# Optimization experiments

Hardware: AMD Instinct MI355X
Metric: run time of the kernel (lower is better)

The kernel has to match this reference:

```python
import jax, jax.numpy as jnp
import numpy as np

B, C3, H3, W3 = 8, 512, 24, 24
C5, H5, W5 = 256, 96, 96
GRIDS = (6, 3, 2, 1)
GROUPS = 2


def conv2d(x, w):
    # stride-1 'same' conv (matches torch autopad k//2 for odd k), NCHW/OIHW
    return jax.lax.conv_general_dilated(x, w, (1, 1), 'SAME',
                                        dimension_numbers=('NCHW', 'OIHW', 'NCHW'))


def conv_bn_silu(x, w):
    # ultralytics-style Conv = Conv2d(bias=False) + BatchNorm2d + SiLU.
    # BN in eval with default running stats (mean=0, var=1, gamma=1, beta=0) is identity.
    return jax.nn.silu(conv2d(x, w))


def psp(x):
    # adaptive_avg_pool2d to (g, g) for each grid; H,W divisible by all grids -> equal bins
    b, c, h, w = x.shape
    outs = []
    for g in GRIDS:
        outs.append(x.reshape(b, c, g, h // g, g, w // g).mean(axis=(3, 5)).reshape(b, c, g * g))
    return jnp.concatenate(outs, axis=2)  # [b, c, 36+9+4+1=50]


def resize_bilinear_ac(x, oh, ow):
    # F.interpolate(mode='bilinear', align_corners=True)
    n, c, h, w = x.shape
    ys = jnp.linspace(0.0, h - 1.0, oh)
    xs = jnp.linspace(0.0, w - 1.0, ow)
    y0 = jnp.clip(jnp.floor(ys).astype(jnp.int32), 0, h - 2)
    x0 = jnp.clip(jnp.floor(xs).astype(jnp.int32), 0, w - 2)
    wy = (ys - y0)[None, None, :, None]
    wx = (xs - x0)[None, None, None, :]
    xr = jnp.take(x, y0, axis=2) * (1 - wy) + jnp.take(x, y0 + 1, axis=2) * wy
    return jnp.take(xr, x0, axis=3) * (1 - wx) + jnp.take(xr, x0 + 1, axis=3) * wx


def grid_sample(img, grid):
    # F.grid_sample bilinear, align_corners=True, padding_mode='zeros'
    # img [N,C,H,W], grid [N,Ho,Wo,2] with (x,y) normalized coords
    n, c, h, w = img.shape
    gx = (grid[..., 0] + 1.0) * 0.5 * (w - 1)
    gy = (grid[..., 1] + 1.0) * 0.5 * (h - 1)
    x0 = jnp.floor(gx)
    y0 = jnp.floor(gy)
    wx1 = gx - x0
    wy1 = gy - y0
    flat = img.reshape(n, c, h * w)

    def gather(xi, yi, wgt):
        valid = (xi >= 0) & (xi <= w - 1) & (yi >= 0) & (yi <= h - 1)
        xc = jnp.clip(xi, 0, w - 1).astype(jnp.int32)
        yc = jnp.clip(yi, 0, h - 1).astype(jnp.int32)
        idx = (yc * w + xc).reshape(n, 1, -1)
        v = jnp.take_along_axis(flat, idx, axis=2).reshape(n, c, grid.shape[1], grid.shape[2])
        return v * (wgt * valid)[:, None]

    return (gather(x0, y0, (1 - wx1) * (1 - wy1)) + gather(x0 + 1, y0, wx1 * (1 - wy1))
            + gather(x0, y0 + 1, (1 - wx1) * wy1) + gather(x0 + 1, y0 + 1, wx1 * wy1))


def _w(key, shape):
    fan_in = int(np.prod(shape[1:]))
    return (jax.random.normal(key, shape, jnp.float32) / np.sqrt(fan_in)).astype(jnp.float32)


def setup_inputs() -> dict:
    key = jax.random.key(0)
    ks = jax.random.split(key, 17)
    return {
        'p3': jax.random.normal(ks[0], (B, C3, H3, W3), jnp.float32),
        'p5': jax.random.normal(ks[1], (B, C5, H5, W5), jnp.float32),
        # CFC_CRB
        'w_red': _w(ks[2], (C3, C3, 3, 3)),
        'wq': _w(ks[3], (32, C3, 1, 1)), 'bq': jnp.zeros((32,), jnp.float32),
        'wk': _w(ks[4], (32, C3)), 'bk': jnp.zeros((32,), jnp.float32),
        'wv': _w(ks[5], (C3, C3)), 'bv': jnp.zeros((C3,), jnp.float32),
        'la_w1': _w(ks[6], (C3 // 8, C3, 1, 1)),
        'la_w2': _w(ks[7], (C3, C3 // 8, 3, 3)),
        # SFC_G2
        'w32': _w(ks[8], (C5, C3, 3, 3)),
        'w8': _w(ks[9], (C5, C5, 3, 3)),
        'woff1': _w(ks[10], (64, 2 * C5, 1, 1)),
        'woff2': _w(ks[11], (GROUPS * 4 + 2, 64, 3, 3)),
    }


def reference(p3, p5, w_red, wq, bq, wk, bk, wv, bv, la_w1, la_w2, w32, w8, woff1, woff2):
    # ---------------- CFC_CRB ----------------
    x = conv_bn_silu(p3, w_red)                      # [b,512,h,w]
    b, c, h, w = x.shape
    q = conv2d(x, wq) + bq[None, :, None, None]       # [b,32,h,w]
    q = q.reshape(b, 32, h * w).transpose(0, 2, 1)    # [b,N,32]
    kfeat = psp(x)                                    # [b,512,50]
    k = jnp.einsum('oc,bcm->bom', wk, kfeat) + bk[None, :, None]   # [b,32,50]
    sim = jax.nn.softmax(jnp.einsum('bnc,bcm->bnm', q, k), axis=-1)  # [b,N,50]
    v = jnp.einsum('oc,bcm->bom', wv, kfeat) + bv[None, :, None]   # [b,512,50]
    context = jnp.einsum('bcm,bnm->bcn', v, sim).reshape(b, c, h, w)
    # LocalAttenModule: res1 * tanh(conv(context)) + res2
    mask = jnp.tanh(conv2d(conv_bn_silu(context, la_w1), la_w2))
    context = context * mask + context
    p3o = x + context                                 # [b,512,24,24]

    # ---------------- SFC_G2 ----------------
    sp = conv_bn_silu(p3o, w32)                       # [b,256,24,24]
    sp = resize_bilinear_ac(sp, H5, W5)               # [b,256,96,96]
    cp = conv_bn_silu(p5, w8)                         # [b,256,96,96]
    cr = conv2d(conv_bn_silu(jnp.concatenate([cp, sp], axis=1), woff1), woff2)  # [b,10,96,96]

    n = b
    spg = sp.reshape(n * GROUPS, -1, H5, W5)
    cpg = cp.reshape(n * GROUPS, -1, H5, W5)
    off_l = cr[:, 0:GROUPS * 2].reshape(n * GROUPS, 2, H5, W5)
    off_h = cr[:, GROUPS * 2:GROUPS * 4].reshape(n * GROUPS, 2, H5, W5)

    gx = jnp.linspace(-1.0, 1.0, W5)
    gy = jnp.linspace(-1.0, 1.0, H5)
    X, Y = jnp.meshgrid(gx, gy)                       # [H5,W5] each
    base = jnp.stack([X, Y], axis=-1)[None]           # [1,H5,W5,2] (x,y)
    norm = jnp.array([W5, H5], dtype=sp.dtype)
    grid_l = base + off_l.transpose(0, 2, 3, 1) / norm
    grid_h = base + off_h.transpose(0, 2, 3, 1) / norm

    cps = grid_sample(cpg, grid_l).reshape(n, -1, H5, W5)
    sps = grid_sample(spg, grid_h).reshape(n, -1, H5, W5)
    att = 1.0 + jnp.tanh(cr[:, GROUPS * 4:])          # [b,2,H,W]
    p5o = sps * att[:, 0:1] + cps * att[:, 1:2]
    return (p3o, p5o)
```

## Files before the change

kernel.cpp:

```cpp
#include <hip/hip_runtime.h>
#include <math.h>

#define DI __device__ __forceinline__

typedef __attribute__((ext_vector_type(8))) short bf16x8;
typedef __attribute__((ext_vector_type(4))) float f32x4;

DI float silu_f(float v) { return v / (1.f + __expf(-v)); }
DI float4 ld4(const float* p) { return *reinterpret_cast<const float4*>(p); }
DI void st4(float* p, const float4& v) { *reinterpret_cast<float4*>(p) = v; }
DI unsigned short f2bf(float f) {
    unsigned u = __float_as_uint(f);
    unsigned r = (u + 0x7FFFu + ((u >> 16) & 1u)) >> 16;
    return (unsigned short)r;
}
DI float bf2f(unsigned short u) { return __uint_as_float(((unsigned)u) << 16); }

DI void gload_lds16(const unsigned short* g, unsigned short* l) {
    __builtin_amdgcn_global_load_lds(
        (const __attribute__((address_space(1))) void*)g,
        (__attribute__((address_space(3))) void*)l, 16, 0, 0);
}

__global__ void pack_w2_kernel(const float* __restrict__ w, unsigned short* __restrict__ pk,
                               int Ci, int Co, int COG) {
    int idx = blockIdx.x * 256 + threadIdx.x;
    int total = Ci * Co * 9;
    if (idx >= total) return;
    int cc = idx & 31;
    int t = idx >> 5;
    int col = t % COG; t /= COG;
    int dydx = t % 9;  t /= 9;
    int nCoG = Co / COG;
    int cog = t % nCoG;
    int ch = t / nCoG;
    int co = cog * COG + col;
    pk[idx] = f2bf(w[((size_t)co * Ci + (ch << 5) + cc) * 9 + dydx]);
}

__global__ void pack_w1_kernel(const float* __restrict__ w, unsigned short* __restrict__ pk) {
    int idx = blockIdx.x * 256 + threadIdx.x;
    if (idx >= 32768) return;
    int cc = idx & 31;
    int col = (idx >> 5) & 63;
    int ch = idx >> 11;
    pk[idx] = f2bf(w[(size_t)col * 512 + (ch << 5) + cc]);
}

__global__ void pack_in_pad_kernel(const float* __restrict__ in, unsigned short* __restrict__ pk,
                                   int Ci, int H, int W, int total) {
    int idx = blockIdx.x * 256 + threadIdx.x;
    if (idx >= total) return;
    const int nCh = Ci >> 5;
    const int HW = H * W;
    int cg = idx & 3;
    int t = idx >> 2;
    int pix = t % HW; t /= HW;
    int ch = t % nCh;
    int b = t / nCh;
    int y = pix / W, x = pix % W;
    const float* src = in + ((size_t)b * Ci + (ch << 5) + (cg << 3)) * HW + pix;
    unsigned p[4];
#pragma unroll
    for (int j = 0; j < 4; ++j) {
        float v0 = src[(size_t)(2 * j) * HW];
        float v1 = src[(size_t)(2 * j + 1) * HW];
        p[j] = (unsigned)f2bf(v0) | ((unsigned)f2bf(v1) << 16);
    }
    size_t dst = (((size_t)b * nCh + ch) * (H + 2) + (y + 1)) * (W + 2) + (x + 1);
    *(uint4*)&pk[dst * 32 + (cg << 3)] = make_uint4(p[0], p[1], p[2], p[3]);
}

template <int TH, int TW, int BF, int WCO, int FUSE, int OUTPK, int OUTPAD>
__global__ void __launch_bounds__(256)
conv3x3_mfma3(const unsigned short* __restrict__ pin, const unsigned short* __restrict__ wpk,
              float* __restrict__ out, unsigned short* __restrict__ outpk,
              int B, int Ci, int Co, int H, int W,
              const float* __restrict__ ctx, const float* __restrict__ xres) {
    static_assert(TH * TW == 4 * BF * 16, "tile px = 4 waves * BF frags * 16");
    constexpr int COG = WCO * 16;
    constexpr int TWH = TW + 2;
    constexpr int HP = (TH + 2) * TWH;
    constexpr int NG = HP * 4;
    constexpr int NIT = (NG + 255) / 256;
    static_assert(NG % 8 == 0, "granules divisible by 8");
    __shared__ __align__(16) unsigned short linA[NG * 8];

    const int nTx = W / TW, nTy = H / TH, nCoG = Co / COG;
    const int Wp = W + 2, Hp = H + 2;
    const int nwg = gridDim.x;
    int wg = (blockIdx.x & 7) * (nwg >> 3) + (blockIdx.x >> 3);
    const int cog = wg % nCoG; wg /= nCoG;
    const int tx = wg % nTx;   wg /= nTx;
    const int ty = wg % nTy;
    const int b = wg / nTy;
    const int ox = tx * TW, oy = ty * TH, co0 = cog * COG;

    const int tid = threadIdx.x;
    const int lane = tid & 63;
    const int l15 = lane & 15, g = lane >> 4;
    const int wpx = (tid >> 6) * (BF * 16);

    int rr[BF], cc_[BF];
#pragma unroll
    for (int bf = 0; bf < BF; ++bf) {
        int px = wpx + bf * 16 + l15;
        rr[bf] = px / TW;
        cc_[bf] = px % TW;
    }

    f32x4 acc[WCO][BF];
#pragma unroll
    for (int af = 0; af < WCO; ++af)
#pragma unroll
        for (int bf = 0; bf < BF; ++bf) acc[af][bf] = {};

    const int nCh = Ci >> 5;
    const size_t HWs = (size_t)H * W;

    for (int ch = 0; ch < nCh; ++ch) {
        {
            const unsigned short* srcb =
                pin + ((size_t)b * nCh + ch) * (size_t)Hp * Wp * 32;
#pragma unroll
            for (int it = 0; it < NIT; ++it) {
                int s = it * 256 + tid;
                if (s < NG) {
                    int e = s ^ ((s >> 3) & 7);
                    int hp = e >> 2, cgp = e & 3;
                    int hy = hp / TWH, hx = hp - hy * TWH;
                    gload_lds16(srcb + ((size_t)(oy + hy) * Wp + (ox + hx)) * 32
                                     + (cgp << 3),
                                &linA[(s & ~63) << 3]);
                }
            }
        }
        __syncthreads();

        {
            const unsigned short* wbase =
                wpk + ((((size_t)ch * nCoG + cog) * 9) * COG + l15) * 32 + (g << 3);
#pragma unroll
            for (int dy = 0; dy < 3; ++dy) {
#pragma unroll
                for (int dx = 0; dx < 3; ++dx) {
                    const int dydx = dy * 3 + dx;
                    bf16x8 a[WCO];
#pragma unroll
                    for (int af = 0; af < WCO; ++af)
                        a[af] = *(const bf16x8*)(wbase + ((size_t)dydx * COG + af * 16) * 32);
                    bf16x8 bb[BF];
#pragma unroll
                    for (int bf = 0; bf < BF; ++bf) {
                        int pxh = (rr[bf] + dy) * TWH + cc_[bf] + dx;
                        int eg = (pxh << 2) | g;
                        int slot = eg ^ ((eg >> 3) & 7);
                        bb[bf] = *(const bf16x8*)&linA[slot << 3];
                    }
#pragma unroll
                    for (int af = 0; af < WCO; ++af)
#pragma unroll
                        for (int bf = 0; bf < BF; ++bf)
                            acc[af][bf] = __builtin_amdgcn_mfma_f32_16x16x32_bf16(
                                a[af], bb[bf], acc[af][bf], 0, 0, 0);
                }
            }
        }
        __syncthreads();
    }

    const int nChO = Co >> 5;
    const size_t opitch = OUTPAD ? (size_t)(H + 2) * (W + 2) : HWs;
#pragma unroll
    for (int af = 0; af < WCO; ++af) {
#pragma unroll
        for (int bf = 0; bf < BF; ++bf) {
            int px = wpx + bf * 16 + l15;
            int y = oy + px / TW, x = ox + px % TW;
            size_t pixg = (size_t)y * W + x;
            int coB = co0 + af * 16 + (g << 2);
            float vv[4];
#pragma unroll
            for (int r4 = 0; r4 < 4; ++r4) {
                float v = acc[af][bf][r4];
                if (FUSE == 1) v = silu_f(v);
                else if (FUSE == 2) {
                    size_t base = ((size_t)b * Co + coB + r4) * HWs + pixg;
                    v = xres[base] + ctx[base] * (1.f + tanhf(v));
                }
                vv[r4] = v;
            }
            if (OUTPK != 1) {
#pragma unroll
                for (int r4 = 0; r4 < 4; ++r4)
                    out[((size_t)b * Co + coB + r4) * HWs + pixg] = vv[r4];
            }
            if (OUTPK >= 1) {
                ushort4 s;
                s.x = f2bf(vv[0]); s.y = f2bf(vv[1]); s.z = f2bf(vv[2]); s.w = f2bf(vv[3]);
                size_t opix = OUTPAD ? ((size_t)(y + 1) * (W + 2) + (x + 1)) : pixg;
                *(ushort4*)&outpk[(((size_t)b * nChO + (coB >> 5)) * opitch + opix) * 32
                                  + (coB & 31)] = s;
            }
        }
    }
}

__global__ void __launch_bounds__(256)
cat_mfma(const unsigned short* __restrict__ cp_pk, const unsigned short* __restrict__ sp_pk,
         const unsigned short* __restrict__ wpk, float* __restrict__ out) {
    __shared__ __align__(16) unsigned short lin1[128 * 36];
    const int nwg = gridDim.x;
    int wg = (blockIdx.x & 7) * (nwg >> 3) + (blockIdx.x >> 3);
    int mt = wg % 72;
    int b = wg / 72;
    int m0 = mt * 128;
    const int tid = threadIdx.x;
    const int wave = tid >> 6, lane = tid & 63;
    const int l15 = lane & 15, g = lane >> 4;
    const int wpx = wave * 32;

    f32x4 acc[4][2];
#pragma unroll
    for (int af = 0; af < 4; ++af)
#pragma unroll
        for (int bf = 0; bf < 2; ++bf) acc[af][bf] = {};

    for (int ch = 0; ch < 16; ++ch) {
        const unsigned short* src = (ch < 8)
            ? cp_pk + (((size_t)b * 8 + ch) * 9216 + m0) * 32
            : sp_pk + (((size_t)b * 8 + ch - 8) * 9216 + m0) * 32;
#pragma unroll
        for (int it = 0; it < 2; ++it) {
            int e = tid + it * 256;
            int px = e >> 2, cg = e & 3;
            *(uint4*)&lin1[px * 36 + (cg << 3)] = *(const uint4*)&src[px * 32 + (cg << 3)];
        }
        __syncthreads();
        const unsigned short* wb = wpk + ((size_t)ch * 64 + l15) * 32 + g * 8;
        bf16x8 a[4];
#pragma unroll
        for (int af = 0; af < 4; ++af)
            a[af] = *(const bf16x8*)(wb + (af * 16) * 32);
        bf16x8 bb[2];
#pragma unroll
        for (int bf = 0; bf < 2; ++bf)
            bb[bf] = *(const bf16x8*)&lin1[(wpx + bf * 16 + l15) * 36 + g * 8];
#pragma unroll
        for (int af = 0; af < 4; ++af)
#pragma unroll
            for (int bf = 0; bf < 2; ++bf)
                acc[af][bf] = __builtin_amdgcn_mfma_f32_16x16x32_bf16(
                    a[af], bb[bf], acc[af][bf], 0, 0, 0);
        __syncthreads();
    }
#pragma unroll
    for (int af = 0; af < 4; ++af) {
#pragma unroll
        for (int bf = 0; bf < 2; ++bf) {
            int m = m0 + wpx + bf * 16 + l15;
#pragma unroll
            for (int r4 = 0; r4 < 4; ++r4) {
                int o = af * 16 + (g << 2) + r4;
                out[((size_t)b * 64 + o) * 9216 + m] = silu_f(acc[af][bf][r4]);
            }
        }
    }
}

DI void gs_params(int x, int y, float ox, float oy, float4* w, int2* p) {
    const float S = 47.5f / 96.f;
    float px = x + ox * S;
    float py = y + oy * S;
    float fx0 = floorf(px), fy0 = floorf(py);
    float wx = px - fx0, wy = py - fy0;
    float vx0 = (fx0 >= 0.f && fx0 <= 95.f) ? 1.f : 0.f;
    float vx1 = (fx0 >= -1.f && fx0 <= 94.f) ? 1.f : 0.f;
    float vy0 = (fy0 >= 0.f && fy0 <= 95.f) ? 1.f : 0.f;
    float vy1 = (fy0 >= -1.f && fy0 <= 94.f) ? 1.f : 0.f;
    int x0 = (int)fminf(fmaxf(fx0, 0.f), 95.f);
    int x1 = (int)fminf(fmaxf(fx0 + 1.f, 0.f), 95.f);
    int y0 = (int)fminf(fmaxf(fy0, 0.f), 95.f);
    int y1 = (int)fminf(fmaxf(fy0 + 1.f, 0.f), 95.f);
    w->x = (1.f - wx) * (1.f - wy) * vx0 * vy0;
    w->y = wx * (1.f - wy) * vx1 * vy0;
    w->z = (1.f - wx) * wy * vx0 * vy1;
    w->w = wx * wy * vx1 * vy1;
    *p = make_int2(x0 | (x1 << 16), y0 | (y1 << 16));
}

template <int TH, int TW, int CO_BLK, int CO_T, int CIC, int FUSE>
__global__ void __launch_bounds__(576)
conv3x3_kernel(const float* __restrict__ in, const float* __restrict__ wgt,
               float* __restrict__ out, int B, int Ci, int Co, int H, int W,
               float4* __restrict__ wpar, int2* __restrict__ ipk,
               float2* __restrict__ attp) {
    constexpr int TWH = TW + 2;
    constexpr int TWP = TW + 3;
    constexpr int SPAT = TH * (TW / 4);
    __shared__ float lin[CIC][TH + 2][TWP];
    __shared__ float wls[CIC][9][CO_BLK];
    __shared__ float crs[10][TH * TW + 1];

    const int nTx = W / TW, nTy = H / TH;
    const int nCoG = (Co + CO_BLK - 1) / CO_BLK;
    int bid = blockIdx.x;
    const int cog = bid % nCoG; bid /= nCoG;
    const int tx = bid % nTx;   bid /= nTx;
    const int ty = bid % nTy;
    const int b = bid / nTy;
    const int ox = tx * TW, oy = ty * TH;
    const int co0 = cog * CO_BLK;

    const int tid = threadIdx.x;
    const int cot = tid / SPAT;
    const int sp = tid % SPAT;
    const int r = sp / (TW / 4);
    const int cg = sp % (TW / 4);

    float acc[4][4];
#pragma unroll
    for (int i = 0; i < 4; ++i)
#pragma unroll
        for (int j = 0; j < 4; ++j) acc[i][j] = 0.f;

    for (int ci0 = 0; ci0 < Ci; ci0 += CIC) {
        for (int e = tid; e < CIC * (TH + 2) * TWH; e += SPAT * CO_T) {
            int xx = e % TWH;
            int yy = (e / TWH) % (TH + 2);
            int cc = e / (TWH * (TH + 2));
            int gy = oy - 1 + yy, gx = ox - 1 + xx;
            float v = 0.f;
            if (gy >= 0 && gy < H && gx >= 0 && gx < W)
                v = in[(((size_t)b * Ci + ci0 + cc) * H + gy) * W + gx];
            lin[cc][yy][xx] = v;
        }
        for (int e = tid; e < CIC * 9 * CO_BLK; e += SPAT * CO_T) {
            int col = e % CO_BLK;
            int k = (e / CO_BLK) % 9;
            int cc = e / (CO_BLK * 9);
            int co = co0 + col;
            float v = 0.f;
            if (co < Co) v = wgt[((size_t)co * Ci + ci0 + cc) * 9 + k];
            wls[cc][k][col] = v;
        }
        __syncthreads();
#pragma unroll
        for (int cc = 0; cc < CIC; ++cc) {
            float v0[3][6];
#pragma unroll
            for (int ky = 0; ky < 3; ++ky)
#pragma unroll
                for (int u = 0; u < 6; ++u)
                    v0[ky][u] = lin[cc][r + ky][cg * 4 + u];
#pragma unroll
            for (int ky = 0; ky < 3; ++ky)
#pragma unroll
                for (int kx = 0; kx < 3; ++kx) {
                    const float4 w4 = ld4(&wls[cc][ky * 3 + kx][cot * 4]);
                    const float wv_[4] = {w4.x, w4.y, w4.z, w4.w};
#pragma unroll
                    for (int i = 0; i < 4; ++i)
#pragma unroll
                        for (int j = 0; j < 4; ++j)
                            acc[i][j] = fmaf(wv_[i], v0[ky][kx + j], acc[i][j]);
                }
        }
        __syncthreads();
    }
    if (FUSE == 3) {
#pragma unroll
        for (int i = 0; i < 4; ++i) {
            int co = co0 + cot * 4 + i;
            if (co >= 10) continue;
#pragma unroll
            for (int j = 0; j < 4; ++j)
                crs[co][r * TW + cg * 4 + j] = acc[i][j];
        }
        __syncthreads();
        for (int e = tid; e < TH * TW; e += SPAT * CO_T) {
            int xx = ox + (e % TW), yy = oy + (e / TW);
            int pixg = yy * 96 + xx;
            float4 w; int2 p;
#pragma unroll
            for (int g2 = 0; g2 < 2; ++g2) {
                gs_params(xx, yy, crs[2 * g2][e], crs[2 * g2 + 1][e], &w, &p);
                size_t el = ((size_t)g2 * 8 + b) * 9216 + pixg;
                wpar[el] = w; ipk[el] = p;
                gs_params(xx, yy, crs[4 + 2 * g2][e], crs[5 + 2 * g2][e], &w, &p);
                size_t eh = ((size_t)(2 + g2) * 8 + b) * 9216 + pixg;
                wpar[eh] = w; ipk[eh] = p;
            }
            float2 at;
            at.x = 1.f + tanhf(crs[8][e]);
            at.y = 1.f + tanhf(crs[9][e]);
            attp[(size_t)b * 9216 + pixg] = at;
        }
    } else {
        const int y = oy + r;
        const int xb = ox + cg * 4;
#pragma unroll
        for (int i = 0; i < 4; ++i) {
            int co = co0 + cot * 4 + i;
            if (co >= Co) continue;
            size_t base = (((size_t)b * Co + co) * H + y) * W + xb;
            float4 res;
            res.x = acc[i][0]; res.y = acc[i][1]; res.z = acc[i][2]; res.w = acc[i][3];
            st4(&out[base], res);
        }
    }
}

template <int ACT, int PK>
__global__ void __launch_bounds__(256)
gemm_om(const float* __restrict__ W, const float* __restrict__ bias,
        const float* __restrict__ in, float* __restrict__ out,
        unsigned short* __restrict__ pko,
        int B, int C, int O, int M, int nOt, int nMt) {
    __shared__ float xs[32][66];
    __shared__ float wls[64][33];
    int bid = blockIdx.x;
    int mt = bid % nMt; bid /= nMt;
    int ot = bid % nOt;
    int b  = bid / nOt;
    int o0 = ot * 64, m0 = mt * 64;
    int tid = threadIdx.x;
    int m_t = tid & 15, o_g = tid >> 4;
    float acc[4][4];
#pragma unroll
    for (int i = 0; i < 4; ++i)
#pragma unroll
        for (int j = 0; j < 4; ++j) acc[i][j] = 0.f;

    for (int c0 = 0; c0 < C; c0 += 32) {
#pragma unroll
        for (int it = 0; it < 8; ++it) {
            int e = tid + it * 256;
            int mm = e & 63, cc = e >> 6;
            float v = 0.f;
            if (m0 + mm < M) v = in[((size_t)b * C + c0 + cc) * M + m0 + mm];
            xs[cc][mm] = v;
        }
#pragma unroll
        for (int it = 0; it < 8; ++it) {
            int e = tid + it * 256;
            int cc = e & 31, ol = e >> 5;
            float v = 0.f;
            if (o0 + ol < O) v = W[(size_t)(o0 + ol) * C + c0 + cc];
            wls[ol][cc] = v;
        }
        __syncthreads();
#pragma unroll
        for (int cc = 0; cc < 32; ++cc) {
            float xv[4], wv[4];
#pragma unroll
            for (int j = 0; j < 4; ++j) xv[j] = xs[cc][j * 16 + m_t];
#pragma unroll
            for (int i = 0; i < 4; ++i) wv[i] = wls[o_g * 4 + i][cc];
#pragma unroll
            for (int i = 0; i < 4; ++i)
#pragma unroll
                for (int j = 0; j < 4; ++j)
                    acc[i][j] = fmaf(wv[i], xv[j], acc[i][j]);
        }
        __syncthreads();
    }
#pragma unroll
    for (int i = 0; i < 4; ++i) {
        int o = o0 + o_g * 4 + i;
        if (o >= O) continue;
        float bv = bias ? bias[o] : 0.f;
#pragma unroll
        for (int j = 0; j < 4; ++j) {
            int m = m0 + j * 16 + m_t;
            if (m >= M) continue;
            float v = acc[i][j] + bv;
            if (ACT == 1) v = silu_f(v);
            if (PK) {
                int yy = m / 24, xx = m % 24;
                pko[(((size_t)b * (O >> 5) + (o >> 5)) * 676
                     + (size_t)(yy + 1) * 26 + (xx + 1)) * 32 + (o & 31)] = f2bf(v);
            } else {
                out[((size_t)b * O + o) * M + m] = v;
            }
        }
    }
}

__global__ void psp_kernel(const float* __restrict__ x, float* __restrict__ kf) {
    __shared__ float pl[576];
    int bc = blockIdx.x;
    const float* xp = x + (size_t)bc * 576;
    for (int e = threadIdx.x; e < 576; e += 64) pl[e] = xp[e];
    __syncthreads();
    int m = threadIdx.x;
    if (m < 50) {
        int g, i0;
        if (m < 36)      { g = 6; i0 = m; }
        else if (m < 45) { g = 3; i0 = m - 36; }
        else if (m < 49) { g = 2; i0 = m - 45; }
        else             { g = 1; i0 = 0; }
        int bs = 24 / g;
        int by = i0 / g, bx = i0 % g;
        float s = 0.f;
        for (int yy = 0; yy < bs; ++yy)
            for (int xx = 0; xx < bs; ++xx)
                s += pl[(by * bs + yy) * 24 + bx * bs + xx];
        kf[(size_t)bc * 50 + m] = s / (float)(bs * bs);
    }
}

__global__ void __launch_bounds__(256)
sim_kernel(const float* __restrict__ q, const float* __restrict__ k,
           float* __restrict__ simg) {
    __shared__ float qs[32][65];
    __shared__ float ks[32][52];
    __shared__ float sm[64][52];
    int b = blockIdx.x / 9, n0 = (blockIdx.x % 9) * 64;
    int tid = threadIdx.x;
    for (int e = tid; e < 32 * 64; e += 256) {
        int c = e >> 6, n = e & 63;
        qs[c][n] = q[((size_t)b * 32 + c) * 576 + n0 + n];
    }
    for (int e = tid; e < 32 * 50; e += 256) {
        int c = e / 50, m = e % 50;
        ks[c][m] = k[((size_t)b * 32 + c) * 50 + m];
    }
    __syncthreads();
    for (int e = tid; e < 64 * 50; e += 256) {
        int n = e / 50, m = e % 50;
        float s = 0.f;
#pragma unroll
        for (int c = 0; c < 32; ++c) s = fmaf(qs[c][n], ks[c][m], s);
        sm[n][m] = s;
    }
    __syncthreads();
    if (tid < 64) {
        float mx = -1e30f;
        for (int m = 0; m < 50; ++m) mx = fmaxf(mx, sm[tid][m]);
        float sum = 0.f;
        for (int m = 0; m < 50; ++m) {
            float e2 = __expf(sm[tid][m] - mx);
            sm[tid][m] = e2;
            sum += e2;
        }
        float inv = 1.f / sum;
        for (int m = 0; m < 50; ++m) sm[tid][m] *= inv;
    }
    __syncthreads();
    for (int e = tid; e < 64 * 50; e += 256) {
        int n = e / 50, m = e % 50;
        simg[((size_t)b * 576 + n0 + n) * 50 + m] = sm[n][m];
    }
}

__global__ void __launch_bounds__(256)
ctx_kernel(const float* __restrict__ v, const float* __restrict__ simg,
           float* __restrict__ ctx) {
    __shared__ float vs[128][54];
    __shared__ float ss[64][54];
    int blk = blockIdx.x;
    int ct = blk & 3; blk >>= 2;
    int nt = blk % 9;
    int b = blk / 9;
    int c0 = ct * 128, n0 = nt * 64;
    int tid = threadIdx.x;
    for (int e = tid; e < 128 * 50; e += 256) {
        int c = e / 50, m = e % 50;
        vs[c][m] = v[((size_t)b * 512 + c0 + c) * 50 + m];
    }
    for (int e = tid; e < 64 * 50; e += 256) {
        int n = e / 50, m = e % 50;
        ss[n][m] = simg[((size_t)b * 576 + n0 + n) * 50 + m];
    }
    __syncthreads();
    int n_t = tid & 15;
    int c_t = tid >> 4;
    float acc[8][4];
#pragma unroll
    for (int i = 0; i < 8; ++i)
#pragma unroll
        for (int j = 0; j < 4; ++j) acc[i][j] = 0.f;
    for (int m = 0; m < 50; ++m) {
        float sv[4];
#pragma unroll
        for (int j = 0; j < 4; ++j) sv[j] = ss[j * 16 + n_t][m];
#pragma unroll
        for (int i = 0; i < 8; ++i) {
            float vv = vs[c_t * 8 + i][m];
#pragma unroll
            for (int j = 0; j < 4; ++j) acc[i][j] = fmaf(vv, sv[j], acc[i][j]);
        }
    }
#pragma unroll
    for (int i = 0; i < 8; ++i)
#pragma unroll
        for (int j = 0; j < 4; ++j)
            ctx[((size_t)b * 512 + c0 + c_t * 8 + i) * 576 + n0 + j * 16 + n_t] = acc[i][j];
}

__global__ void upsample2_kernel(const float* __restrict__ in, unsigned short* __restrict__ outpk) {
    int idx = blockIdx.x * 256 + threadIdx.x;
    if (idx >= 8 * 8 * 4 * 9216) return;
    int cg = idx & 3;
    int t = idx >> 2;
    int pix = t % 9216; t /= 9216;
    int ch = t & 7;
    int b = t >> 3;
    int x = pix % 96, y = pix / 96;
    float fy = y * (23.f / 95.f);
    float fx = x * (23.f / 95.f);
    int y0 = (int)fy; if (y0 > 22) y0 = 22;
    int x0 = (int)fx; if (x0 > 22) x0 = 22;
    float wy = fy - y0, wx = fx - x0;
    const float* base = in + ((size_t)b * 256 + ch * 32 + cg * 8) * 576 + y0 * 24 + x0;
    unsigned short s[8];
#pragma unroll
    for (int j = 0; j < 8; ++j) {
        const float* ip = base + (size_t)j * 576;
        float a = ip[0], bb = ip[1], c = ip[24], d = ip[25];
        float l = a * (1.f - wy) + c * wy;
        float r = bb * (1.f - wy) + d * wy;
        s[j] = f2bf(l * (1.f - wx) + r * wx);
    }
    *(uint4*)&outpk[(((size_t)b * 8 + ch) * 9216 + pix) * 32 + cg * 8] =
        make_uint4((unsigned)s[0] | ((unsigned)s[1] << 16),
                   (unsigned)s[2] | ((unsigned)s[3] << 16),
                   (unsigned)s[4] | ((unsigned)s[5] << 16),
                   (unsigned)s[6] | ((unsigned)s[7] << 16));
}

__global__ void __launch_bounds__(256)
gsample3_kernel(const unsigned short* __restrict__ cp_pk, const unsigned short* __restrict__ sp_pk,
                const float4* __restrict__ wpar, const int2* __restrict__ ipk,
                const float2* __restrict__ attp, float* __restrict__ p5o) {
    int idx = blockIdx.x * 256 + threadIdx.x;
    if (idx >= 8 * 32 * 9216) return;
    int pix = idx % 9216;
    int cb = (idx / 9216) & 31;
    int b = idx / (9216 * 32);
    int c0 = cb * 8;
    int g = c0 >> 7, ch = c0 >> 5, coff = c0 & 31;
    size_t el = ((size_t)g * 8 + b) * 9216 + pix;
    size_t eh = ((size_t)(2 + g) * 8 + b) * 9216 + pix;
    float4 wl = wpar[el]; int2 pl = ipk[el];
    float4 wh = wpar[eh]; int2 ph = ipk[eh];
    float2 at = attp[(size_t)b * 9216 + pix];
    int l00 = (pl.y & 0xffff) * 96 + (pl.x & 0xffff);
    int l01 = (pl.y & 0xffff) * 96 + (pl.x >> 16);
    int l10 = (pl.y >> 16) * 96 + (pl.x & 0xffff);
    int l11 = (pl.y >> 16) * 96 + (pl.x >> 16);
    int h00 = (ph.y & 0xffff) * 96 + (ph.x & 0xffff);
    int h01 = (ph.y & 0xffff) * 96 + (ph.x >> 16);
    int h10 = (ph.y >> 16) * 96 + (ph.x & 0xffff);
    int h11 = (ph.y >> 16) * 96 + (ph.x >> 16);
    const unsigned short* cb0 = cp_pk + (((size_t)b * 8 + ch) * 9216) * 32 + coff;
    const unsigned short* sb0 = sp_pk + (((size_t)b * 8 + ch) * 9216) * 32 + coff;
    ushort4 tc0 = *(const ushort4*)&cb0[(size_t)l00 * 32];
    ushort4 tc0b = *(const ushort4*)&cb0[(size_t)l00 * 32 + 4];
    ushort4 tc1 = *(const ushort4*)&cb0[(size_t)l01 * 32];
    ushort4 tc1b = *(const ushort4*)&cb0[(size_t)l01 * 32 + 4];
    ushort4 tc2 = *(const ushort4*)&cb0[(size_t)l10 * 32];
    ushort4 tc2b = *(const ushort4*)&cb0[(size_t)l10 * 32 + 4];
    ushort4 tc3 = *(const ushort4*)&cb0[(size_t)l11 * 32];
    ushort4 tc3b = *(const ushort4*)&cb0[(size_t)l11 * 32 + 4];
    ushort4 ts0 = *(const ushort4*)&sb0[(size_t)h00 * 32];
    ushort4 ts0b = *(const ushort4*)&sb0[(size_t)h00 * 32 + 4];
    ushort4 ts1 = *(const ushort4*)&sb0[(size_t)h01 * 32];
    ushort4 ts1b = *(const ushort4*)&sb0[(size_t)h01 * 32 + 4];
    ushort4 ts2 = *(const ushort4*)&sb0[(size_t)h10 * 32];
    ushort4 ts2b = *(const ushort4*)&sb0[(size_t)h10 * 32 + 4];
    ushort4 ts3 = *(const ushort4*)&sb0[(size_t)h11 * 32];
    ushort4 ts3b = *(const ushort4*)&sb0[(size_t)h11 * 32 + 4];
    const unsigned short* c0a = (const unsigned short*)&tc0;
    const unsigned short* c0bp = (const unsigned short*)&tc0b;
    const unsigned short* c1a = (const unsigned short*)&tc1;
    const unsigned short* c1bp = (const unsigned short*)&tc1b;
    const unsigned short* c2a = (const unsigned short*)&tc2;
    const unsigned short* c2bp = (const unsigned short*)&tc2b;
    const unsigned short* c3a = (const unsigned short*)&tc3;
    const unsigned short* c3bp = (const unsigned short*)&tc3b;
    const unsigned short* s0a = (const unsigned short*)&ts0;
    const unsigned short* s0bp = (const unsigned short*)&ts0b;
    const unsigned short* s1a = (const unsigned short*)&ts1;
    const unsigned short* s1bp = (const unsigned short*)&ts1b;
    const unsigned short* s2a = (const unsigned short*)&ts2;
    const unsigned short* s2bp = (const unsigned short*)&ts2b;
    const unsigned short* s3a = (const unsigned short*)&ts3;
    const unsigned short* s3bp = (const unsigned short*)&ts3b;
    float* op = p5o + ((size_t)b * 256 + c0) * 9216 + pix;
#pragma unroll
    for (int i = 0; i < 8; ++i) {
        unsigned short v0 = (i < 4) ? c0a[i] : c0bp[i - 4];
        unsigned short v1 = (i < 4) ? c1a[i] : c1bp[i - 4];
        unsigned short v2 = (i < 4) ? c2a[i] : c2bp[i - 4];
        unsigned short v3 = (i < 4) ? c3a[i] : c3bp[i - 4];
        float cps = wl.x * bf2f(v0) + wl.y * bf2f(v1) + wl.z * bf2f(v2) + wl.w * bf2f(v3);
        unsigned short u0 = (i < 4) ? s0a[i] : s0bp[i - 4];
        unsigned short u1 = (i < 4) ? s1a[i] : s1bp[i - 4];
        unsigned short u2 = (i < 4) ? s2a[i] : s2bp[i - 4];
        unsigned short u3 = (i < 4) ? s3a[i] : s3bp[i - 4];
        float sps = wh.x * bf2f(u0) + wh.y * bf2f(u1) + wh.z * bf2f(u2) + wh.w * bf2f(u3);
        op[(size_t)i * 9216] = sps * at.x + cps * at.y;
    }
}

extern "C" void kernel_launch(void* const* d_in, const int* in_sizes, int n_in,
                              void* d_out, int out_size, void* d_ws, size_t ws_size,
                              hipStream_t stream) {
    const float* p3    = (const float*)d_in[0];
    const float* p5    = (const float*)d_in[1];
    const float* w_red = (const float*)d_in[2];
    const float* wq    = (const float*)d_in[3];
    const float* bq    = (const float*)d_in[4];
    const float* wk    = (const float*)d_in[5];
    const float* bk    = (const float*)d_in[6];
    const float* wv    = (const float*)d_in[7];
    const float* bv    = (const float*)d_in[8];
    const float* la_w1 = (const float*)d_in[9];
    const float* la_w2 = (const float*)d_in[10];
    const float* w32   = (const float*)d_in[11];
    const float* w8    = (const float*)d_in[12];
    const float* woff1 = (const float*)d_in[13];
    const float* woff2 = (const float*)d_in[14];

    float* out = (float*)d_out;
    float* p3o = out;
    float* p5o = out + 2359296;

    float* ws = (float*)d_ws;
    float* x_   = ws + 0;
    float* ctx  = ws + 2359296;
    float* q    = ws + 4718592;
    float* kf   = ws + 4866048;
    float* km   = ws + 5070848;
    float* vm   = ws + 5083648;
    unsigned short* la1_pk = (unsigned short*)(ws + 5288448);
    float* sp24 = ws + 5461504;
    float4* wpar = (float4*)(ws + 6641152);
    int2*   ipk  = (int2*)(ws + 7820800);
    float2* attp = (float2*)(ws + 8410624);
    float* simg = ws + 8558080;
    unsigned short* sp96_pk = (unsigned short*)(ws + 8788480);
    unsigned short* cp_pk   = (unsigned short*)(ws + 18225664);
    unsigned short* p5_pk   = (unsigned short*)(ws + 27662848);
    unsigned short* p3_pk   = (unsigned short*)(ws + 37497344);
    unsigned short* wred_pk = (unsigned short*)(ws + 38881792);
    unsigned short* w32_pk  = (unsigned short*)(ws + 40061440);
    unsigned short* w8_pk   = (unsigned short*)(ws + 40651264);
    unsigned short* wla2_pk = (unsigned short*)(ws + 40946176);
    unsigned short* woff1_pk= (unsigned short*)(ws + 41093632);
    float* t64  = ws + 0;

    hipMemsetAsync(p5_pk, 0, (size_t)8 * 8 * 98 * 98 * 32 * 2, stream);
    hipMemsetAsync(p3_pk, 0, (size_t)8 * 16 * 676 * 32 * 2, stream);
    hipMemsetAsync(la1_pk, 0, (size_t)8 * 2 * 676 * 32 * 2, stream);

    pack_w2_kernel<<<dim3(2359296 / 256), dim3(256), 0, stream>>>(w_red, wred_pk, 512, 512, 32);
    pack_w2_kernel<<<dim3(1179648 / 256), dim3(256), 0, stream>>>(w32, w32_pk, 512, 256, 16);
    pack_w2_kernel<<<dim3(589824 / 256), dim3(256), 0, stream>>>(w8, w8_pk, 256, 256, 64);
    pack_w2_kernel<<<dim3(294912 / 256), dim3(256), 0, stream>>>(la_w2, wla2_pk, 64, 512, 32);
    pack_w1_kernel<<<dim3(128), dim3(256), 0, stream>>>(woff1, woff1_pk);
    pack_in_pad_kernel<<<dim3(9216), dim3(256), 0, stream>>>(p5, p5_pk, 256, 96, 96, 2359296);
    pack_in_pad_kernel<<<dim3(1152), dim3(256), 0, stream>>>(p3, p3_pk, 512, 24, 24, 294912);

    conv3x3_mfma3<16, 16, 4, 4, 1, 1, 0><<<dim3(1152), dim3(256), 0, stream>>>(
        p5_pk, w8_pk, nullptr, cp_pk, 8, 256, 256, 96, 96, nullptr, nullptr);
    conv3x3_mfma3<8, 24, 3, 2, 1, 0, 0><<<dim3(384), dim3(256), 0, stream>>>(
        p3_pk, wred_pk, x_, nullptr, 8, 512, 512, 24, 24, nullptr, nullptr);
    gemm_om<0, 0><<<dim3(72), dim3(256), 0, stream>>>(
        wq, bq, x_, q, nullptr, 8, 512, 32, 576, 1, 9);
    psp_kernel<<<dim3(8 * 512), dim3(64), 0, stream>>>(x_, kf);
    gemm_om<0, 0><<<dim3(8), dim3(256), 0, stream>>>(
        wk, bk, kf, km, nullptr, 8, 512, 32, 50, 1, 1);
    gemm_om<0, 0><<<dim3(64), dim3(256), 0, stream>>>(
        wv, bv, kf, vm, nullptr, 8, 512, 512, 50, 8, 1);
    sim_kernel<<<dim3(72), dim3(256), 0, stream>>>(q, km, simg);
    ctx_kernel<<<dim3(288), dim3(256), 0, stream>>>(vm, simg, ctx);
    gemm_om<1, 1><<<dim3(72), dim3(256), 0, stream>>>(
        la_w1, nullptr, ctx, nullptr, la1_pk, 8, 512, 64, 576, 1, 9);
    conv3x3_mfma3<8, 24, 3, 2, 2, 2, 1><<<dim3(384), dim3(256), 0, stream>>>(
        la1_pk, wla2_pk, p3o, p3_pk, 8, 64, 512, 24, 24, ctx, x_);
    conv3x3_mfma3<8, 24, 3, 1, 1, 0, 0><<<dim3(384), dim3(256), 0, stream>>>(
        p3_pk, w32_pk, sp24, nullptr, 8, 512, 256, 24, 24, nullptr, nullptr);
    upsample2_kernel<<<dim3(9216), dim3(256), 0, stream>>>(sp24, sp96_pk);
    cat_mfma<<<dim3(576), dim3(256), 0, stream>>>(cp_pk, sp96_pk, woff1_pk, t64);
    conv3x3_kernel<8, 32, 12, 3, 4, 3><<<dim3(288), dim3(192), 0, stream>>>(
        t64, woff2, nullptr, 8, 64, 10, 96, 96, wpar, ipk, attp);
    gsample3_kernel<<<dim3(9216), dim3(256), 0, stream>>>(
        cp_pk, sp96_pk, wpar, ipk, attp, p5o);
}
```

Baseline: 857.3 us.

## Double-buffer conv LDS staging, store cat output as bf16, fuse K/V projections

Adds an optional double-buffered LDS pipeline to the MFMA 3x3 conv and turns it on for the large 96x96 cp conv, so global-to-LDS loads for the next channel chunk overlap compute on the current one. The cat_mfma output is now written as packed bf16 in channel-blocked layout, and the following offset conv reads that layout, which halves intermediate traffic. The separate K and V projection GEMMs are merged into one gemm_kv launch. These trade extra LDS use, which can lower occupancy, and bf16 rounding of the intermediate for fewer memory stalls and fewer launches.

```diff
diff --git a/kernel.cpp b/kernel.cpp
--- a/kernel.cpp
+++ b/kernel.cpp
@@ -71,7 +71,7 @@
     *(uint4*)&pk[dst * 32 + (cg << 3)] = make_uint4(p[0], p[1], p[2], p[3]);
 }
 
-template <int TH, int TW, int BF, int WCO, int FUSE, int OUTPK, int OUTPAD>
+template <int TH, int TW, int BF, int WCO, int FUSE, int OUTPK, int OUTPAD, int DBUF>
 __global__ void __launch_bounds__(256)
 conv3x3_mfma3(const unsigned short* __restrict__ pin, const unsigned short* __restrict__ wpk,
               float* __restrict__ out, unsigned short* __restrict__ outpk,
@@ -84,7 +84,7 @@
     constexpr int NG = HP * 4;
     constexpr int NIT = (NG + 255) / 256;
     static_assert(NG % 8 == 0, "granules divisible by 8");
-    __shared__ __align__(16) unsigned short linA[NG * 8];
+    __shared__ __align__(16) unsigned short lin[NG * 8 * (DBUF + 1)];
 
     const int nTx = W / TW, nTy = H / TH, nCoG = Co / COG;
     const int Wp = W + 2, Hp = H + 2;
@@ -117,56 +117,69 @@
 
     const int nCh = Ci >> 5;
     const size_t HWs = (size_t)H * W;
-
-    for (int ch = 0; ch < nCh; ++ch) {
-        {
-            const unsigned short* srcb =
-                pin + ((size_t)b * nCh + ch) * (size_t)Hp * Wp * 32;
-#pragma unroll
-            for (int it = 0; it < NIT; ++it) {
-                int s = it * 256 + tid;
-                if (s < NG) {
-                    int e = s ^ ((s >> 3) & 7);
-                    int hp = e >> 2, cgp = e & 3;
-                    int hy = hp / TWH, hx = hp - hy * TWH;
-                    gload_lds16(srcb + ((size_t)(oy + hy) * Wp + (ox + hx)) * 32
-                                     + (cgp << 3),
-                                &linA[(s & ~63) << 3]);
+    const size_t HpWp = (size_t)Hp * Wp;
+
+    auto stage = [&](int ch, int buf) {
+        const unsigned short* srcb = pin + ((size_t)b * nCh + ch) * HpWp * 32;
+        unsigned short* dst = lin + buf * (NG * 8);
+#pragma unroll
+        for (int it = 0; it < NIT; ++it) {
+            int s = it * 256 + tid;
+            if (s < NG) {
+                int e = s ^ ((s >> 3) & 7);
+                int hp = e >> 2, cgp = e & 3;
+                int hy = hp / TWH, hx = hp - hy * TWH;
+                gload_lds16(srcb + ((size_t)(oy + hy) * Wp + (ox + hx)) * 32 + (cgp << 3),
+                            &dst[(s & ~63) << 3]);
+            }
+        }
+    };
+    auto compute = [&](int ch, int buf) {
+        const unsigned short* src = lin + buf * (NG * 8);
+        const unsigned short* wbase =
+            wpk + ((((size_t)ch * nCoG + cog) * 9) * COG + l15) * 32 + (g << 3);
+#pragma unroll
+        for (int dy = 0; dy < 3; ++dy) {
+#pragma unroll
+            for (int dx = 0; dx < 3; ++dx) {
+                const int dydx = dy * 3 + dx;
+                bf16x8 a[WCO];
+#pragma unroll
+                for (int af = 0; af < WCO; ++af)
+                    a[af] = *(const bf16x8*)(wbase + ((size_t)dydx * COG + af * 16) * 32);
+                bf16x8 bb[BF];
+#pragma unroll
+                for (int bf = 0; bf < BF; ++bf) {
+                    int pxh = (rr[bf] + dy) * TWH + cc_[bf] + dx;
+                    int eg = (pxh << 2) | g;
+                    int slot = eg ^ ((eg >> 3) & 7);
+                    bb[bf] = *(const bf16x8*)&src[slot << 3];
                 }
+#pragma unroll
+                for (int af = 0; af < WCO; ++af)
+#pragma unroll
+                    for (int bf = 0; bf < BF; ++bf)
+                        acc[af][bf] = __builtin_amdgcn_mfma_f32_16x16x32_bf16(
+                            a[af], bb[bf], acc[af][bf], 0, 0, 0);
             }
         }
-        __syncthreads();
-
-        {
-            const unsigned short* wbase =
-                wpk + ((((size_t)ch * nCoG + cog) * 9) * COG + l15) * 32 + (g << 3);
-#pragma unroll
-            for (int dy = 0; dy < 3; ++dy) {
-#pragma unroll
-                for (int dx = 0; dx < 3; ++dx) {
-                    const int dydx = dy * 3 + dx;
-                    bf16x8 a[WCO];
-#pragma unroll
-                    for (int af = 0; af < WCO; ++af)
-                        a[af] = *(const bf16x8*)(wbase + ((size_t)dydx * COG + af * 16) * 32);
-                    bf16x8 bb[BF];
-#pragma unroll
-                    for (int bf = 0; bf < BF; ++bf) {
-                        int pxh = (rr[bf] + dy) * TWH + cc_[bf] + dx;
-                        int eg = (pxh << 2) | g;
-                        int slot = eg ^ ((eg >> 3) & 7);
-                        bb[bf] = *(const bf16x8*)&linA[slot << 3];
-                    }
-#pragma unroll
-                    for (int af = 0; af < WCO; ++af)
-#pragma unroll
-                        for (int bf = 0; bf < BF; ++bf)
-                            acc[af][bf] = __builtin_amdgcn_mfma_f32_16x16x32_bf16(
-                                a[af], bb[bf], acc[af][bf], 0, 0, 0);
-                }
-            }
-        }
-        __syncthreads();
+    };
+
+    if (DBUF) {
+        stage(0, 0);
+        __syncthreads();
+        for (int ch = 0; ch < nCh; ++ch) {
+            if (ch + 1 < nCh) stage(ch + 1, (ch + 1) & 1);
+            compute(ch, ch & 1);
+            __syncthreads();
+        }
+    } else {
+        for (int ch = 0; ch < nCh; ++ch) {
+            stage(ch, 0);
+            __syncthreads();
+            compute(ch, 0);
+            __syncthreads();
+        }
     }
 
     const int nChO = Co >> 5;
@@ -208,7 +221,7 @@
 
 __global__ void __launch_bounds__(256)
 cat_mfma(const unsigned short* __restrict__ cp_pk, const unsigned short* __restrict__ sp_pk,
-         const unsigned short* __restrict__ wpk, float* __restrict__ out) {
+         const unsigned short* __restrict__ wpk, unsigned short* __restrict__ outpk) {
     __shared__ __align__(16) unsigned short lin1[128 * 36];
     const int nwg = gridDim.x;
     int wg = (blockIdx.x & 7) * (nwg >> 3) + (blockIdx.x >> 3);
@@ -259,11 +272,13 @@
 #pragma unroll
         for (int bf = 0; bf < 2; ++bf) {
             int m = m0 + wpx + bf * 16 + l15;
-#pragma unroll
-            for (int r4 = 0; r4 < 4; ++r4) {
-                int o = af * 16 + (g << 2) + r4;
-                out[((size_t)b * 64 + o) * 9216 + m] = silu_f(acc[af][bf][r4]);
-            }
+            int o = af * 16 + (g << 2);
+            ushort4 s;
+            s.x = f2bf(silu_f(acc[af][bf][0]));
+            s.y = f2bf(silu_f(acc[af][bf][1]));
+            s.z = f2bf(silu_f(acc[af][bf][2]));
+            s.w = f2bf(silu_f(acc[af][bf][3]));
+            *(ushort4*)&outpk[(((size_t)b * 2 + (o >> 5)) * 9216 + m) * 32 + (o & 31)] = s;
         }
     }
 }
@@ -291,7 +306,7 @@
 
 template <int TH, int TW, int CO_BLK, int CO_T, int CIC, int FUSE>
 __global__ void __launch_bounds__(576)
-conv3x3_kernel(const float* __restrict__ in, const float* __restrict__ wgt,
+conv3x3_kernel(const unsigned short* __restrict__ in, const float* __restrict__ wgt,
                float* __restrict__ out, int B, int Ci, int Co, int H, int W,
                float4* __restrict__ wpar, int2* __restrict__ ipk,
                float2* __restrict__ attp) {
@@ -317,6 +332,7 @@
     const int sp = tid % SPAT;
     const int r = sp / (TW / 4);
     const int cg = sp % (TW / 4);
+    const int nChI = Ci >> 5;
 
     float acc[4][4];
 #pragma unroll
@@ -331,8 +347,11 @@
             int cc = e / (TWH * (TH + 2));
             int gy = oy - 1 + yy, gx = ox - 1 + xx;
             float v = 0.f;
-            if (gy >= 0 && gy < H && gx >= 0 && gx < W)
-                v = in[(((size_t)b * Ci + ci0 + cc) * H + gy) * W + gx];
+            if (gy >= 0 && gy < H && gx >= 0 && gx < W) {
+                int ci = ci0 + cc;
+                v = bf2f(in[(((size_t)b * nChI + (ci >> 5)) * H * W
+                             + (size_t)gy * W + gx) * 32 + (ci & 31)]);
+            }
             lin[cc][yy][xx] = v;
         }
         for (int e = tid; e < CIC * 9 * CO_BLK; e += SPAT * CO_T) {
@@ -483,6 +502,74 @@
             } else {
                 out[((size_t)b * O + o) * M + m] = v;
             }
+        }
+    }
+}
+
+__global__ void __launch_bounds__(256)
+gemm_kv(const float* __restrict__ wk, const float* __restrict__ bk,
+        const float* __restrict__ wv, const float* __restrict__ bv,
+        const float* __restrict__ in, float* __restrict__ kv) {
+    __shared__ float xs[32][66];
+    __shared__ float wls[64][33];
+    const int O = 544, M = 50, C = 512;
+    int bid = blockIdx.x;
+    int ot = bid % 9;
+    int b  = bid / 9;
+    int o0 = ot * 64;
+    int tid = threadIdx.x;
+    int m_t = tid & 15, o_g = tid >> 4;
+    float acc[4][4];
+#pragma unroll
+    for (int i = 0; i < 4; ++i)
+#pragma unroll
+        for (int j = 0; j < 4; ++j) acc[i][j] = 0.f;
+
+    for (int c0 = 0; c0 < C; c0 += 32) {
+#pragma unroll
+        for (int it = 0; it < 8; ++it) {
+            int e = tid + it * 256;
+            int mm = e & 63, cc = e >> 6;
+            float v = 0.f;
+            if (mm < M) v = in[((size_t)b * C + c0 + cc) * M + mm];
+            xs[cc][mm] = v;
+        }
+#pragma unroll
+        for (int it = 0; it < 8; ++it) {
+            int e = tid + it * 256;
+            int cc = e & 31, ol = e >> 5;
+            int o = o0 + ol;
+            float v = 0.f;
+            if (o < 32) v = wk[(size_t)o * C + c0 + cc];
+            else if (o < O) v = wv[(size_t)(o - 32) * C + c0 + cc];
+            wls[ol][cc] = v;
+        }
+        __syncthreads();
+#pragma unroll
+        for (int cc = 0; cc < 32; ++cc) {
+            float xv[4], wv_[4];
+#pragma unroll
+            for (int j = 0; j < 4; ++j) xv[j] = xs[cc][j * 16 + m_t];
+#pragma unroll
+            for (int i = 0; i < 4; ++i) wv_[i] = wls[o_g * 4 + i][cc];
+#pragma unroll
+            for (int i = 0; i < 4; ++i)
+#pragma unroll
+                for (int j = 0; j < 4; ++j)
+                    acc[i][j] = fmaf(wv_[i], xv[j], acc[i][j]);
+        }
+        __syncthreads();
+    }
+#pragma unroll
+    for (int i = 0; i < 4; ++i) {
+        int o = o0 + o_g * 4 + i;
+        if (o >= O) continue;
+        float bvv = (o < 32) ? bk[o] : bv[o - 32];
+#pragma unroll
+        for (int j = 0; j < 4; ++j) {
+            int m = j * 16 + m_t;
+            if (m >= M) continue;
+            kv[((size_t)b * O + o) * M + m] = acc[i][j] + bvv;
         }
     }
 }
@@ -511,7 +598,7 @@
 }
 
 __global__ void __launch_bounds__(256)
-sim_kernel(const float* __restrict__ q, const float* __restrict__ k,
+sim_kernel(const float* __restrict__ q, const float* __restrict__ kv,
            float* __restrict__ simg) {
     __shared__ float qs[32][65];
     __shared__ float ks[32][52];
@@ -524,7 +611,7 @@
     }
     for (int e = tid; e < 32 * 50; e += 256) {
         int c = e / 50, m = e % 50;
-        ks[c][m] = k[((size_t)b * 32 + c) * 50 + m];
+        ks[c][m] = kv[((size_t)b * 544 + c) * 50 + m];
     }
     __syncthreads();
     for (int e = tid; e < 64 * 50; e += 256) {
@@ -555,7 +642,7 @@
 }
 
 __global__ void __launch_bounds__(256)
-ctx_kernel(const float* __restrict__ v, const float* __restrict__ simg,
+ctx_kernel(const float* __restrict__ kv, const float* __restrict__ simg,
            float* __restrict__ ctx) {
     __shared__ float vs[128][54];
     __shared__ float ss[64][54];
@@ -567,7 +654,7 @@
     int tid = threadIdx.x;
     for (int e = tid; e < 128 * 50; e += 256) {
         int c = e / 50, m = e % 50;
-        vs[c][m] = v[((size_t)b * 512 + c0 + c) * 50 + m];
+        vs[c][m] = kv[((size_t)b * 544 + 32 + c0 + c) * 50 + m];
     }
     for (int e = tid; e < 64 * 50; e += 256) {
         int n = e / 50, m = e % 50;
@@ -733,8 +820,7 @@
     float* ctx  = ws + 2359296;
     float* q    = ws + 4718592;
     float* kf   = ws + 4866048;
-    float* km   = ws + 5070848;
-    float* vm   = ws + 5083648;
+    float* kv   = ws + 5070848;
     unsigned short* la1_pk = (unsigned short*)(ws + 5288448);
     float* sp24 = ws + 5461504;
     float4* wpar = (float4*)(ws + 6641152);
@@ -750,7 +836,7 @@
     unsigned short* w8_pk   = (unsigned short*)(ws + 40651264);
     unsigned short* wla2_pk = (unsigned short*)(ws + 40946176);
     unsigned short* woff1_pk= (unsigned short*)(ws + 41093632);
-    float* t64  = ws + 0;
+    unsigned short* t64_pk  = (unsigned short*)(ws + 0);
 
     hipMemsetAsync(p5_pk, 0, (size_t)8 * 8 * 98 * 98 * 32 * 2, stream);
     hipMemsetAsync(p3_pk, 0, (size_t)8 * 16 * 676 * 32 * 2, stream);
@@ -764,29 +850,26 @@
     pack_in_pad_kernel<<<dim3(9216), dim3(256), 0, stream>>>(p5, p5_pk, 256, 96, 96, 2359296);
     pack_in_pad_kernel<<<dim3(1152), dim3(256), 0, stream>>>(p3, p3_pk, 512, 24, 24, 294912);
 
-    conv3x3_mfma3<16, 16, 4, 4, 1, 1, 0><<<dim3(1152), dim3(256), 0, stream>>>(
+    conv3x3_mfma3<16, 16, 4, 4, 1, 1, 0, 1><<<dim3(1152), dim3(256), 0, stream>>>(
         p5_pk, w8_pk, nullptr, cp_pk, 8, 256, 256, 96, 96, nullptr, nullptr);
-    conv3x3_mfma3<8, 24, 3, 2, 1, 0, 0><<<dim3(384), dim3(256), 0, stream>>>(
+    conv3x3_mfma3<8, 24, 3, 2, 1, 0, 0, 0><<<dim3(384), dim3(256), 0, stream>>>(
         p3_pk, wred_pk, x_, nullptr, 8, 512, 512, 24, 24, nullptr, nullptr);
     gemm_om<0, 0><<<dim3(72), dim3(256), 0, stream>>>(
         wq, bq, x_, q, nullptr, 8, 512, 32, 576, 1, 9);
     psp_kernel<<<dim3(8 * 512), dim3(64), 0, stream>>>(x_, kf);
-    gemm_om<0, 0><<<dim3(8), dim3(256), 0, stream>>>(
-        wk, bk, kf, km, nullptr, 8, 512, 32, 50, 1, 1);
-    gemm_om<0, 0><<<dim3(64), dim3(256), 0, stream>>>(
-        wv, bv, kf, vm, nullptr, 8, 512, 512, 50, 8, 1);
-    sim_kernel<<<dim3(72), dim3(256), 0, stream>>>(q, km, simg);
-    ctx_kernel<<<dim3(288), dim3(256), 0, stream>>>(vm, simg, ctx);
+    gemm_kv<<<dim3(72), dim3(256), 0, stream>>>(wk, bk, wv, bv, kf, kv);
+    sim_kernel<<<dim3(72), dim3(256), 0, stream>>>(q, kv, simg);
+    ctx_kernel<<<dim3(288), dim3(256), 0, stream>>>(kv, simg, ctx);
     gemm_om<1, 1><<<dim3(72), dim3(256), 0, stream>>>(
         la_w1, nullptr, ctx, nullptr, la1_pk, 8, 512, 64, 576, 1, 9);
-    conv3x3_mfma3<8, 24, 3, 2, 2, 2, 1><<<dim3(384), dim3(256), 0, stream>>>(
+    conv3x3_mfma3<8, 24, 3, 2, 2, 2, 1, 0><<<dim3(384), dim3(256), 0, stream>>>(
         la1_pk, wla2_pk, p3o, p3_pk, 8, 64, 512, 24, 24, ctx, x_);
-    conv3x3_mfma3<8, 24, 3, 1, 1, 0, 0><<<dim3(384), dim3(256), 0, stream>>>(
+    conv3x3_mfma3<8, 24, 3, 1, 1, 0, 0, 0><<<dim3(384), dim3(256), 0, stream>>>(
         p3_pk, w32_pk, sp24, nullptr, 8, 512, 256, 24, 24, nullptr, nullptr);
     upsample2_kernel<<<dim3(9216), dim3(256), 0, stream>>>(sp24, sp96_pk);
-    cat_mfma<<<dim3(576), dim3(256), 0, stream>>>(cp_pk, sp96_pk, woff1_pk, t64);
+    cat_mfma<<<dim3(576), dim3(256), 0, stream>>>(cp_pk, sp96_pk, woff1_pk, t64_pk);
     conv3x3_kernel<8, 32, 12, 3, 4, 3><<<dim3(288), dim3(192), 0, stream>>>(
-        t64, woff2, nullptr, 8, 64, 10, 96, 96, wpar, ipk, attp);
+        t64_pk, woff2, nullptr, 8, 64, 10, 96, 96, wpar, ipk, attp);
     gsample3_kernel<<<dim3(9216), dim3(256), 0, stream>>>(
         cp_pk, sp96_pk, wpar, ipk, attp, p5o);
 }
```

Measured after the change: 825.7 us. 3.7% less time.
